# Kernel optimization log

Measured on AMD Instinct MI355X. Metric: run time of the kernel, lower is better.

Reference implementation:

```python
import jax, jax.numpy as jnp
import numpy as np
from jax import lax

V_PATCH = (1, 2, 3, 4, 5, 6, 8, 10, 13, 16)
BETA = 0.25
RESI = 0.5          # abs(quant_resi): h*(1-r) + conv(h)*r
K_PHI = 4           # share_quant_resi
PHI_TICKS = np.linspace(1.0 / (3 * K_PHI), 1.0 - 1.0 / (3 * K_PHI), K_PHI)


def _area_mat(out_s, in_s):
    # torch F.interpolate(mode='area') == adaptive avg pool: row-stochastic matrix
    M = np.zeros((out_s, in_s), np.float32)
    for i in range(out_s):
        s = (i * in_s) // out_s
        e = -((-(i + 1) * in_s) // out_s)  # ceil((i+1)*in/out)
        M[i, s:e] = 1.0 / (e - s)
    return jnp.asarray(M)


def _bicubic_mat(out_s, in_s):
    # torch bicubic, align_corners=False, a=-0.75, border-clamped taps
    a = -0.75
    i = np.arange(out_s)
    src = (i + 0.5) * in_s / out_s - 0.5
    fl = np.floor(src)
    M = np.zeros((out_s, in_s), np.float32)
    for t in range(-1, 3):
        x = np.abs(src - (fl + t))
        w = np.where(x <= 1.0, (a + 2) * x**3 - (a + 3) * x**2 + 1.0,
                     np.where(x < 2.0, a * x**3 - 5 * a * x**2 + 8 * a * x - 4 * a, 0.0))
        idx = np.clip(fl + t, 0, in_s - 1).astype(int)
        np.add.at(M, (i, idx), w)
    return jnp.asarray(M)


def _resize(x, M):
    # separable resize on square maps: x [B,C,h,w] -> [B,C,o,o]
    x = jnp.einsum('oh,bchw->bcow', M, x)
    return jnp.einsum('pw,bcow->bcop', M, x)


def _phi(h, w, b):
    # Phi: Conv2d(C,C,3,pad=1); out = h*(1-r) + conv(h)*r
    c = lax.conv_general_dilated(h, w, (1, 1), 'SAME',
                                 dimension_numbers=('NCHW', 'OIHW', 'NCHW'))
    c = c + b[None, :, None, None]
    return h * (1.0 - RESI) + c * RESI


def setup_inputs() -> dict:
    key = jax.random.key(0)
    k1, k2, k3, k4 = jax.random.split(key, 4)
    f = jax.random.normal(k1, (128, 32, 16, 16), jnp.float32)
    emb = jax.random.normal(k2, (4096, 32), jnp.float32) * 0.1
    phi_w = jax.random.normal(k3, (4, 32, 32, 3, 3), jnp.float32) * 0.05
    phi_b = jax.random.normal(k4, (4, 32), jnp.float32) * 0.01
    return {"f_BChw": f, "emb_W": emb, "phi_W": phi_w, "phi_b": phi_b}


def reference(f_BChw, emb_W, phi_W, phi_b):
    B, C, H, W = f_BChw.shape
    SN = len(V_PATCH)
    f = f_BChw.astype(jnp.float32)
    f_ng = lax.stop_gradient(f)
    f_rest = f_ng
    f_hat = jnp.zeros_like(f_ng)
    emb_ng = lax.stop_gradient(emb_W)         # torch uses embedding.weight.data
    e_sq = jnp.sum(emb_ng**2, axis=1)          # [V]
    loss = jnp.float32(0.0)
    idx_list = []
    for si, pn in enumerate(V_PATCH):
        rest = f_rest if si == SN - 1 else _resize(f_rest, _area_mat(pn, H))
        rest_NC = rest.transpose(0, 2, 3, 1).reshape(-1, C)      # [B*pn*pn, C]
        d = jnp.sum(rest_NC**2, axis=1, keepdims=True) + e_sq - 2.0 * (rest_NC @ emb_ng.T)
        idx = jnp.argmin(d, axis=1)                              # [B*pn*pn]
        idx_list.append(idx)
        h = emb_W[idx].reshape(B, pn, pn, C).transpose(0, 3, 1, 2)  # differentiable gather
        if si != SN - 1:
            h = _resize(h, _bicubic_mat(H, pn))
        k = int(np.argmin(np.abs(PHI_TICKS - si / (SN - 1))))
        h = _phi(h, phi_W[k], phi_b[k])
        f_hat = f_hat + h
        f_rest = f_rest - h
        loss = loss + BETA * jnp.mean((lax.stop_gradient(f_hat) - f)**2) \
                    + jnp.mean((f_hat - f_ng)**2)
    loss = loss / SN
    f_hat_out = lax.stop_gradient(f_hat) - f_ng + f  # straight-through
    return (f_hat_out, loss, jnp.concatenate(idx_list))
```

## Files before the change

kernel.cpp:

```cpp
#include <hip/hip_runtime.h>
#include <hip/hip_bf16.h>
#include <math.h>


#define B_  128
#define V_  4096
#define SN_ 10
#define NPIX_ (B_*32*256)

#define WS_FREST   0
#define WS_PD      1048576
#define WS_PI      1310720
#define WS_ESQ     1572864
#define WS_TW      1576960
#define WS_TI      1577536
#define WS_LOSSP   1578112
#define WS_RESTH   1580672
#define WS_RESTM   2104960
#define WS_RESTL   2629248
#define WS_EMBH    3153536
#define WS_EMBM    3219072
#define WS_EMBL    3284608
#define WS_WSPL    3350144

typedef __attribute__((ext_vector_type(8))) short short8_t;
typedef __attribute__((ext_vector_type(4))) float f32x4;
#define MFMA(a,b,c) __builtin_amdgcn_mfma_f32_16x16x32_bf16((a),(b),(c),0,0,0)

__device__ inline void gl_lds16(const void* g, void* l) {
  __builtin_amdgcn_global_load_lds((const __attribute__((address_space(1))) void*)g,
                                   (__attribute__((address_space(3))) void*)l, 16, 0, 0);
}
__device__ inline void gl_lds4(const void* g, void* l) {
  __builtin_amdgcn_global_load_lds((const __attribute__((address_space(1))) void*)g,
                                   (__attribute__((address_space(3))) void*)l, 4, 0, 0);
}

__device__ inline void split3(float a, ushort* h, ushort* m, ushort* l) {
  unsigned ua = __float_as_uint(a);
  ushort uh = (ushort)(ua >> 16);
  float fh = __uint_as_float((unsigned)uh << 16);
  float r1 = a - fh;
  ushort um = (ushort)(__float_as_uint(r1) >> 16);
  float fm = __uint_as_float((unsigned)um << 16);
  float r2 = r1 - fm;
  ushort ul = (ushort)(__float_as_uint(r2) >> 16);
  *h = uh; *m = um; *l = ul;
}

__device__ inline short8_t s8_from_laneM1(short8_t v) {
  union { short8_t s; unsigned u[4]; } a, r;
  a.s = v;
#pragma unroll
  for (int i = 0; i < 4; ++i)
    r.u[i] = __builtin_amdgcn_update_dpp(0u, a.u[i], 0x111, 0xF, 0xF, true);
  return r.s;
}
__device__ inline short8_t s8_from_laneP1(short8_t v) {
  union { short8_t s; unsigned u[4]; } a, r;
  a.s = v;
#pragma unroll
  for (int i = 0; i < 4; ++i)
    r.u[i] = __builtin_amdgcn_update_dpp(0u, a.u[i], 0x101, 0xF, 0xF, true);
  return r.s;
}


__global__ __launch_bounds__(256) void k_prep(const float* __restrict__ emb,
                                              const float* __restrict__ f,
                                              const float* __restrict__ phiW,
                                              float* __restrict__ esq,
                                              ushort* __restrict__ eh,
                                              ushort* __restrict__ em,
                                              ushort* __restrict__ el,
                                              float* __restrict__ tw,
                                              int* __restrict__ ti,
                                              ushort* __restrict__ rh,
                                              ushort* __restrict__ rm,
                                              ushort* __restrict__ rl,
                                              ushort* __restrict__ wspl) {
  int bx = blockIdx.x, t = threadIdx.x;
  if (bx < 16) {
    int v = bx * 256 + t;
    const float4* e4 = (const float4*)(emb + (size_t)v * 32);
    float s = 0.f;
#pragma unroll
    for (int half = 0; half < 4; ++half) {
      float4 x0 = e4[half * 2], x1 = e4[half * 2 + 1];
      s += x0.x * x0.x + x0.y * x0.y + x0.z * x0.z + x0.w * x0.w;
      s += x1.x * x1.x + x1.y * x1.y + x1.z * x1.z + x1.w * x1.w;
      float xs[8] = {x0.x, x0.y, x0.z, x0.w, x1.x, x1.y, x1.z, x1.w};
      ushort hs[8], ms[8], ls[8];
#pragma unroll
      for (int j = 0; j < 8; ++j) split3(xs[j], &hs[j], &ms[j], &ls[j]);
      uint4 ph, pm, pl;
      ph.x = (unsigned)hs[0] | ((unsigned)hs[1] << 16); ph.y = (unsigned)hs[2] | ((unsigned)hs[3] << 16);
      ph.z = (unsigned)hs[4] | ((unsigned)hs[5] << 16); ph.w = (unsigned)hs[6] | ((unsigned)hs[7] << 16);
      pm.x = (unsigned)ms[0] | ((unsigned)ms[1] << 16); pm.y = (unsigned)ms[2] | ((unsigned)ms[3] << 16);
      pm.z = (unsigned)ms[4] | ((unsigned)ms[5] << 16); pm.w = (unsigned)ms[6] | ((unsigned)ms[7] << 16);
      pl.x = (unsigned)ls[0] | ((unsigned)ls[1] << 16); pl.y = (unsigned)ls[2] | ((unsigned)ls[3] << 16);
      pl.z = (unsigned)ls[4] | ((unsigned)ls[5] << 16); pl.w = (unsigned)ls[6] | ((unsigned)ls[7] << 16);
      ((uint4*)(eh + (size_t)v * 32))[half] = ph;
      ((uint4*)(em + (size_t)v * 32))[half] = pm;
      ((uint4*)(el + (size_t)v * 32))[half] = pl;
    }
    esq[v] = -0.5f * s;
  } else if (bx == 16) {
    if (t >= 144) return;
    const int pns[9] = {1, 2, 3, 4, 5, 6, 8, 10, 13};
    int si = t / 16, Y = t % 16;
    int pn = pns[si];
    double src = (Y + 0.5) * (double)pn / 16.0 - 0.5;
    double fl = floor(src);
    const double a = -0.75;
#pragma unroll
    for (int k = 0; k < 4; ++k) {
      double x = fabs(src - (fl + (k - 1)));
      double w;
      if (x <= 1.0)      w = (a + 2.0) * x * x * x - (a + 3.0) * x * x + 1.0;
      else if (x < 2.0)  w = a * x * x * x - 5.0 * a * x * x + 8.0 * a * x - 4.0 * a;
      else               w = 0.0;
      int id = (int)fl + (k - 1);
      id = id < 0 ? 0 : (id > pn - 1 ? pn - 1 : id);
      tw[si * 64 + Y * 4 + k] = (float)w;
      ti[si * 64 + Y * 4 + k] = id;
    }
  } else if (bx < 33) {
    int i = (bx - 17) * 256 + t;
    int phi = i >> 10, o = (i >> 5) & 31, ci = i & 31;
    const float* src = phiW + (((size_t)phi * 32 + o) * 32 + ci) * 9;
    ushort* dst = wspl + (size_t)phi * 27648;
#pragma unroll
    for (int q = 0; q < 9; ++q) {
      ushort uh, um, ul;
      split3(src[q], &uh, &um, &ul);
      dst[(size_t)(0 * 9 + q) * 1024 + o * 32 + ci] = uh;
      dst[(size_t)(9 + q) * 1024 + o * 32 + ci] = um;
      dst[(size_t)(18 + q) * 1024 + o * 32 + ci] = ul;
    }
  } else {
    int tid = (bx - 33) * 256 + t;
    int c = tid & 31, n = tid >> 5;
    const float* base = f + ((size_t)n * 32 + c) * 256;
    float s = 0.f;
    for (int yy = 0; yy < 16; ++yy)
      for (int xx = 0; xx < 16; ++xx) s += base[yy * 16 + xx];
    float a = s * ((1.0f / 16.0f) * (1.0f / 16.0f));
    ushort uh, um, ul;
    split3(a, &uh, &um, &ul);
    rh[(size_t)n * 32 + c] = uh;
    rm[(size_t)n * 32 + c] = um;
    rl[(size_t)n * 32 + c] = ul;
  }
}

template<int R>
__global__ __launch_bounds__(256) void k_nn(const ushort* __restrict__ rest_h,
                                            const ushort* __restrict__ rest_m,
                                            const ushort* __restrict__ rest_l,
                                            const ushort* __restrict__ emb_h,
                                            const ushort* __restrict__ emb_m,
                                            const ushort* __restrict__ emb_l,
                                            const float* __restrict__ esq_g,
                                            float* __restrict__ pdist,
                                            int* __restrict__ pidx,
                                            int rows, int S, int cps) {
  __shared__ ushort lb[3][3][2048];
  __shared__ float les[3][64];
  const int t = threadIdx.x;
  const int w = t >> 6;
  const int col = t & 15;
  const int g = (t >> 4) & 3;
  const int sp = blockIdx.y;
  const int rowbase = blockIdx.x * (64 * R);

  auto stage = [&](int bf, int ch) {
    int cb = sp * cps + ch * 64;
    int code = cb + (t >> 2);
    int u = (t & 3) ^ ((code ^ (code >> 2)) & 3);
    size_t off = (size_t)code * 32 + (size_t)u * 8;
    gl_lds16(emb_h + off, &lb[bf][0][w * 512]);
    gl_lds16(emb_m + off, &lb[bf][1][w * 512]);
    gl_lds16(emb_l + off, &lb[bf][2][w * 512]);
    if ((t & 63) < 16) gl_lds4(esq_g + cb + w * 16 + (t & 15), &les[bf][w * 16]);
  };

  const int NC = cps >> 6;
  stage(0, 0);

  short8_t ah[R], am[R], al[R];
#pragma unroll
  for (int rt = 0; rt < R; ++rt) {
    int n = rowbase + (w * R + rt) * 16 + col;
    if (n >= rows) n = rows - 1;
    size_t o = (size_t)n * 32 + g * 8;
    ah[rt] = *(const short8_t*)(rest_h + o);
    am[rt] = *(const short8_t*)(rest_m + o);
    al[rt] = *(const short8_t*)(rest_l + o);
  }

  if (NC > 1) stage(1, 1);

  float best[R][4];
  int bidx[R][4];
#pragma unroll
  for (int rt = 0; rt < R; ++rt)
#pragma unroll
    for (int r = 0; r < 4; ++r) { best[rt][r] = -3.4e38f; bidx[rt][r] = 0x7fffffff; }

  int buf = 0;
  for (int ch = 0; ch < NC; ++ch) {
    if (ch + 2 < NC) {
      stage((ch + 2) % 3, ch + 2);
      asm volatile("s_waitcnt vmcnt(8)" ::: "memory");
    } else if (ch + 1 < NC) {
      asm volatile("s_waitcnt vmcnt(4)" ::: "memory");
    } else {
      asm volatile("s_waitcnt vmcnt(0)" ::: "memory");
    }
    __builtin_amdgcn_s_barrier();

    int cb0 = sp * cps + ch * 64;
#pragma unroll
    for (int s4 = 0; s4 < 4; ++s4) {
      int cl = s4 * 16 + col;
      int slotbase = (cl * 4 + (g ^ ((cl ^ (cl >> 2)) & 3))) * 8;
      short8_t bh  = *(const short8_t*)&lb[buf][0][slotbase];
      short8_t bm  = *(const short8_t*)&lb[buf][1][slotbase];
      short8_t bl2 = *(const short8_t*)&lb[buf][2][slotbase];
      float es = les[buf][cl];
      f32x4 c0 = {es, es, es, es};
      f32x4 acc[R];
#pragma unroll
      for (int rt = 0; rt < R; ++rt) acc[rt] = MFMA(ah[rt], bh, c0);
#pragma unroll
      for (int rt = 0; rt < R; ++rt) acc[rt] = MFMA(ah[rt], bm, acc[rt]);
#pragma unroll
      for (int rt = 0; rt < R; ++rt) acc[rt] = MFMA(am[rt], bh, acc[rt]);
#pragma unroll
      for (int rt = 0; rt < R; ++rt) acc[rt] = MFMA(ah[rt], bl2, acc[rt]);
#pragma unroll
      for (int rt = 0; rt < R; ++rt) acc[rt] = MFMA(am[rt], bm, acc[rt]);
#pragma unroll
      for (int rt = 0; rt < R; ++rt) acc[rt] = MFMA(al[rt], bh, acc[rt]);
      int code = cb0 + cl;
#pragma unroll
      for (int rt = 0; rt < R; ++rt)
#pragma unroll
        for (int r = 0; r < 4; ++r)
          if (acc[rt][r] > best[rt][r]) { best[rt][r] = acc[rt][r]; bidx[rt][r] = code; }
    }
    __syncthreads();
    buf = (buf + 1) % 3;
  }

#pragma unroll
  for (int rt = 0; rt < R; ++rt)
#pragma unroll
    for (int r = 0; r < 4; ++r) {
      float bd = best[rt][r];
      int bi = bidx[rt][r];
#pragma unroll
      for (int mm2 = 1; mm2 < 16; mm2 <<= 1) {
        float od = __shfl_xor(bd, mm2, 16);
        int oi = __shfl_xor(bi, mm2, 16);
        if (od > bd || (od == bd && oi < bi)) { bd = od; bi = oi; }
      }
      if ((t & 15) == 0) {
        int rown = rowbase + (w * R + rt) * 16 + g * 4 + r;
        if (rown < rows) {
          pdist[(size_t)rown * S + sp] = bd;
          pidx[(size_t)rown * S + sp] = bi;
        }
      }
    }
}

template<bool LAST>
__global__ __launch_bounds__(512) void k_scale(const float* __restrict__ pdist,
                                               const int* __restrict__ pidx,
                                               const float* __restrict__ emb,
                                               const float* __restrict__ tw,
                                               const int* __restrict__ ti,
                                               const ushort* __restrict__ wspl,
                                               const float* __restrict__ bias,
                                               const float* __restrict__ f,
                                               const float* __restrict__ fr_in,
                                               float* __restrict__ fr_out,
                                               float* __restrict__ fhat_out,
                                               float* __restrict__ out_idx_f,
                                               float* __restrict__ lossp,
                                               ushort* __restrict__ rh,
                                               ushort* __restrict__ rm,
                                               ushort* __restrict__ rl,
                                               int S, int pn, int si, int pn_next) {
  __shared__ ushort h_bf[3][256][40];
  __shared__ float xt[32][208];
  __shared__ float h_my[16][260];
  __shared__ int ci_s[256];
  __shared__ float redw[8];
  float* hsm = (float*)&h_bf[0][0][0];
  float* poolb = &xt[0][0];

  const int b = blockIdx.x;
  const int cog = blockIdx.y * 16;
  const int t = threadIdx.x;
  const int pn2 = pn * pn;

  for (int rem = t; rem < pn2; rem += 512) {
    const float* pd = pdist + (size_t)(b * pn2 + rem) * S;
    const int* pi = pidx + (size_t)(b * pn2 + rem) * S;
    float bd = pd[0]; int bi = pi[0];
    for (int s = 1; s < S; ++s) {
      float d = pd[s]; int i2 = pi[s];
      if (d > bd || (d == bd && i2 < bi)) { bd = d; bi = i2; }
    }
    ci_s[rem] = bi;
    out_idx_f[b * pn2 + rem] = (float)bi;
  }
  __syncthreads();

  if (LAST) {
    for (int i = t; i < 8192; i += 512) {
      int pix = i & 255, c = i >> 8;
      float v = emb[(size_t)ci_s[pix] * 32 + c];
      ushort uh, um, ul; split3(v, &uh, &um, &ul);
      h_bf[0][pix][c] = uh; h_bf[1][pix][c] = um; h_bf[2][pix][c] = ul;
      int cl = c - cog;
      if ((unsigned)cl < 16u) h_my[cl][pix] = v;
    }
  } else {
    for (int i = t; i < 32 * pn2; i += 512) {
      int c = i & 31, rem = i >> 5;
      hsm[c * 176 + rem] = emb[(size_t)ci_s[rem] * 32 + c];
    }
    __syncthreads();
    int e1 = 32 * pn * 16;
    for (int i = t; i < e1; i += 512) {
      int X = i & 15, r2 = i >> 4;
      int y = r2 % pn, c = r2 / pn;
      float a = 0.f;
#pragma unroll
      for (int u = 0; u < 4; ++u)
        a += tw[si * 64 + X * 4 + u] * hsm[c * 176 + y * pn + ti[si * 64 + X * 4 + u]];
      xt[c][y * 16 + X] = a;
    }
    __syncthreads();
    for (int i = t; i < 8192; i += 512) {
      int pix = i & 255, c = i >> 8;
      int X = pix & 15, Y = pix >> 4;
      float a = 0.f;
#pragma unroll
      for (int u = 0; u < 4; ++u)
        a += tw[si * 64 + Y * 4 + u] * xt[c][ti[si * 64 + Y * 4 + u] * 16 + X];
      ushort uh, um, ul; split3(a, &uh, &um, &ul);
      h_bf[0][pix][c] = uh; h_bf[1][pix][c] = um; h_bf[2][pix][c] = ul;
      int cl = c - cog;
      if ((unsigned)cl < 16u) h_my[cl][pix] = a;
    }
  }
  __syncthreads();

  const int w = t >> 6, l = t & 63;
  const int X = l & 15, kq = l >> 4;

  float fr_old[2][4], f_old[2][4];
#pragma unroll
  for (int rr = 0; rr < 2; ++rr) {
    int pix = (w * 2 + rr) * 16 + X;
#pragma unroll
    for (int r = 0; r < 4; ++r) {
      size_t ga = ((size_t)b * 32 + cog + kq * 4 + r) * 256 + pix;
      fr_old[rr][r] = fr_in[ga];
      f_old[rr][r] = LAST ? f[ga] : 0.f;
    }
  }

  f32x4 accA[2], accB[2];
#pragma unroll
  for (int r = 0; r < 4; ++r) {
    float bv = bias[cog + kq * 4 + r];
    accA[0][r] = bv; accA[1][r] = bv;
    accB[0][r] = 0.f; accB[1][r] = 0.f;
  }

  for (int dy = 0; dy < 3; ++dy) {
    short8_t bc[2][3];
    bool ok0, ok1;
    {
      int Yp = w * 2 + 0 + dy - 1;
      ok0 = (Yp >= 0 && Yp < 16);
      if (ok0) {
#pragma unroll
        for (int lv = 0; lv < 3; ++lv)
          bc[0][lv] = *(const short8_t*)&h_bf[lv][Yp * 16 + X][kq * 8];
      }
    }
    {
      int Yp = w * 2 + 1 + dy - 1;
      ok1 = (Yp >= 0 && Yp < 16);
      if (ok1) {
#pragma unroll
        for (int lv = 0; lv < 3; ++lv)
          bc[1][lv] = *(const short8_t*)&h_bf[lv][Yp * 16 + X][kq * 8];
      }
    }
#pragma unroll
    for (int dx = 0; dx < 3; ++dx) {
      int q = dy * 3 + dx;
      const ushort* wp = wspl + (size_t)q * 1024 + (size_t)(cog + (l & 15)) * 32 + kq * 8;
      short8_t aH = *(const short8_t*)(wp);
      short8_t aM = *(const short8_t*)(wp + 9 * 1024);
      short8_t aL = *(const short8_t*)(wp + 18 * 1024);
#pragma unroll
      for (int rr = 0; rr < 2; ++rr) {
        bool ok = rr ? ok1 : ok0;
        if (!ok) continue;
        short8_t bH = bc[rr][0], bM = bc[rr][1], bL = bc[rr][2];
        if (dx == 0) { bH = s8_from_laneM1(bH); bM = s8_from_laneM1(bM); bL = s8_from_laneM1(bL); }
        else if (dx == 2) { bH = s8_from_laneP1(bH); bM = s8_from_laneP1(bM); bL = s8_from_laneP1(bL); }
        accA[rr] = MFMA(aH, bH, accA[rr]);
        accB[rr] = MFMA(aH, bM, accB[rr]);
        accA[rr] = MFMA(aM, bH, accA[rr]);
        accB[rr] = MFMA(aH, bL, accB[rr]);
        accA[rr] = MFMA(aM, bM, accA[rr]);
        accB[rr] = MFMA(aL, bH, accB[rr]);
      }
    }
  }

  float lsum = 0.f;
#pragma unroll
  for (int rr = 0; rr < 2; ++rr) {
    int pix = (w * 2 + rr) * 16 + X;
#pragma unroll
    for (int r = 0; r < 4; ++r) {
      int ol = kq * 4 + r;
      float convv = accA[rr][r] + accB[rr][r];
      float outv = 0.5f * h_my[ol][pix] + 0.5f * convv;
      float nf = fr_old[rr][r] - outv;
      size_t ga = ((size_t)b * 32 + cog + ol) * 256 + pix;
      if (LAST) {
        fhat_out[ga] = f_old[rr][r] - nf;
      } else {
        fr_out[ga] = nf;
        poolb[ol * 256 + pix] = nf;
      }
      lsum += nf * nf;
    }
  }

  if (!LAST) {
    __syncthreads();
    int pn2n = pn_next * pn_next;
    for (int i = t; i < 16 * pn2n; i += 512) {
      int o = i / pn2n, rem = i - o * pn2n;
      int y = rem / pn_next, x = rem - y * pn_next;
      int sy = (y * 16) / pn_next, ey = ((y + 1) * 16 + pn_next - 1) / pn_next;
      int sx = (x * 16) / pn_next, ex = ((x + 1) * 16 + pn_next - 1) / pn_next;
      float s = 0.f;
      for (int yy = sy; yy < ey; ++yy)
        for (int xx = sx; xx < ex; ++xx) s += poolb[o * 256 + yy * 16 + xx];
      float a = s * ((1.0f / (float)(ey - sy)) * (1.0f / (float)(ex - sx)));
      ushort uh, um, ul;
      split3(a, &uh, &um, &ul);
      size_t n = (size_t)b * pn2n + rem;
      rh[n * 32 + cog + o] = uh;
      rm[n * 32 + cog + o] = um;
      rl[n * 32 + cog + o] = ul;
    }
  }

#pragma unroll
  for (int off = 32; off > 0; off >>= 1) lsum += __shfl_down(lsum, off);
  if (l == 0) redw[w] = lsum;
  __syncthreads();
  if (t == 0) {
    float s2 = 0.f;
#pragma unroll
    for (int i = 0; i < 8; ++i) s2 += redw[i];
    lossp[si * 256 + blockIdx.y * 128 + b] = s2;
  }
}

__global__ __launch_bounds__(256) void k_lossfin(const float* __restrict__ part,
                                                 float* __restrict__ out) {
  int t = threadIdx.x;
  float s = 0.f;
  for (int i = t; i < SN_ * 256; i += 256) s += part[i];
  __shared__ float red[256];
  red[t] = s;
  __syncthreads();
  for (int o = 128; o > 0; o >>= 1) {
    if (t < o) red[t] += red[t + o];
    __syncthreads();
  }
  if (t == 0) out[NPIX_] = red[0] * (1.25f / (10.0f * (float)NPIX_));
}


static void compute_phi_k(int* ks) {
  const int K = 4;
  double start = 1.0 / (3.0 * K);
  double stop = 1.0 - 1.0 / (3.0 * K);
  double step = (stop - start) / (K - 1);
  double ticks[4];
  for (int i = 0; i < K; ++i) ticks[i] = (double)i * step + start;
  ticks[K - 1] = stop;
  for (int si = 0; si < SN_; ++si) {
    double x = (double)si / (SN_ - 1);
    int best = 0;
    double bd = fabs(ticks[0] - x);
    for (int i = 1; i < K; ++i) {
      double d = fabs(ticks[i] - x);
      if (d < bd) { bd = d; best = i; }
    }
    ks[si] = best;
  }
}

extern "C" void kernel_launch(void* const* d_in, const int* in_sizes, int n_in,
                              void* d_out, int out_size, void* d_ws, size_t ws_size,
                              hipStream_t stream) {
  (void)in_sizes; (void)n_in; (void)out_size; (void)ws_size;
  const float* f    = (const float*)d_in[0];
  const float* emb  = (const float*)d_in[1];
  const float* phiW = (const float*)d_in[2];
  const float* phiB = (const float*)d_in[3];
  float* out = (float*)d_out;
  float* ws = (float*)d_ws;

  float* f_rest = ws + WS_FREST;
  float* pdist  = ws + WS_PD;
  int*   pidx   = (int*)(ws + WS_PI);
  float* esq    = ws + WS_ESQ;
  float* tw     = ws + WS_TW;
  int*   ti     = (int*)(ws + WS_TI);
  float* lossp  = ws + WS_LOSSP;
  ushort* rest_h = (ushort*)(ws + WS_RESTH);
  ushort* rest_m = (ushort*)(ws + WS_RESTM);
  ushort* rest_l = (ushort*)(ws + WS_RESTL);
  ushort* emb_h  = (ushort*)(ws + WS_EMBH);
  ushort* emb_m  = (ushort*)(ws + WS_EMBM);
  ushort* emb_l  = (ushort*)(ws + WS_EMBL);
  ushort* wspl   = (ushort*)(ws + WS_WSPL);

  static const int pns[SN_] = {1, 2, 3, 4, 5, 6, 8, 10, 13, 16};
  static const int Rs[SN_]  = {1, 1, 1, 2, 2, 2, 4, 4, 4, 4};
  static const int Ss[SN_]  = {64, 64, 32, 32, 32, 16, 16, 16, 8, 8};
  int ks[SN_];
  compute_phi_k(ks);

  k_prep<<<49, 256, 0, stream>>>(emb, f, phiW, esq, emb_h, emb_m, emb_l, tw, ti,
                                 rest_h, rest_m, rest_l, wspl);

  int idx_off = 0;
  for (int si = 0; si < SN_; ++si) {
    int pn = pns[si];
    int pn2 = pn * pn;
    int rows = B_ * pn2;
    int R = Rs[si], S = Ss[si];
    int cps = V_ / S;
    int rowblocks = (rows + 64 * R - 1) / (64 * R);

    dim3 grid(rowblocks, S);
    if (R == 1)
      k_nn<1><<<grid, 256, 0, stream>>>(rest_h, rest_m, rest_l, emb_h, emb_m, emb_l,
                                        esq, pdist, pidx, rows, S, cps);
    else if (R == 2)
      k_nn<2><<<grid, 256, 0, stream>>>(rest_h, rest_m, rest_l, emb_h, emb_m, emb_l,
                                        esq, pdist, pidx, rows, S, cps);
    else
      k_nn<4><<<grid, 256, 0, stream>>>(rest_h, rest_m, rest_l, emb_h, emb_m, emb_l,
                                        esq, pdist, pidx, rows, S, cps);

    bool last = (si == SN_ - 1);
    int pn_next = last ? 0 : pns[si + 1];
    const ushort* wsp = wspl + (size_t)ks[si] * 27648;
    const float* bi = phiB + (size_t)ks[si] * 32;
    if (last)
      k_scale<true><<<dim3(B_, 2), 512, 0, stream>>>(
          pdist, pidx, emb, tw, ti, wsp, bi, f,
          f_rest, f_rest, out,
          out + NPIX_ + 1 + idx_off, lossp,
          rest_h, rest_m, rest_l, S, pn, si, pn_next);
    else
      k_scale<false><<<dim3(B_, 2), 512, 0, stream>>>(
          pdist, pidx, emb, tw, ti, wsp, bi, f,
          (si == 0) ? f : f_rest, f_rest, nullptr,
          out + NPIX_ + 1 + idx_off, lossp,
          rest_h, rest_m, rest_l, S, pn, si, pn_next);
    idx_off += rows;
  }

  k_lossfin<<<1, 256, 0, stream>>>(lossp, out);
}
```

Measured before the change: 425.3 us.

## Widen k_scale to 1024 threads, stage conv weights in LDS, raise NN splits

k_scale now runs 1024 threads, with one image row per wave instead of two. The 3x3 conv weight slices for the block's 16 output channels are staged once into LDS rather than re-read from global memory inside the dy/dx loop. The nearest-neighbour kernel uses more codebook splits (S) and smaller R at mid scales, which raises grid parallelism, and it raises wave priority around the MFMA chain. The risks are larger partial-result buffers (the workspace layout is shifted to fit them), more LDS per block, and extra partial entries to reduce in k_scale.

Result: slower. 463.5 us (+9.0%).

```diff
diff --git a/kernel.cpp b/kernel.cpp
--- a/kernel.cpp
+++ b/kernel.cpp
@@ -10,18 +10,18 @@
 
 #define WS_FREST   0
 #define WS_PD      1048576
-#define WS_PI      1310720
-#define WS_ESQ     1572864
-#define WS_TW      1576960
-#define WS_TI      1577536
-#define WS_LOSSP   1578112
-#define WS_RESTH   1580672
-#define WS_RESTM   2104960
-#define WS_RESTL   2629248
-#define WS_EMBH    3153536
-#define WS_EMBM    3219072
-#define WS_EMBL    3284608
-#define WS_WSPL    3350144
+#define WS_PI      1572864
+#define WS_ESQ     2097152
+#define WS_TW      2101248
+#define WS_TI      2101824
+#define WS_LOSSP   2102400
+#define WS_RESTH   2105344
+#define WS_RESTM   2629632
+#define WS_RESTL   3153920
+#define WS_EMBH    3678208
+#define WS_EMBM    3743744
+#define WS_EMBL    3809280
+#define WS_WSPL    3874816
 
 typedef __attribute__((ext_vector_type(8))) short short8_t;
 typedef __attribute__((ext_vector_type(4))) float f32x4;
@@ -231,6 +231,7 @@
       float es = les[buf][cl];
       f32x4 c0 = {es, es, es, es};
       f32x4 acc[R];
+      __builtin_amdgcn_s_setprio(1);
 #pragma unroll
       for (int rt = 0; rt < R; ++rt) acc[rt] = MFMA(ah[rt], bh, c0);
 #pragma unroll
@@ -243,6 +244,7 @@
       for (int rt = 0; rt < R; ++rt) acc[rt] = MFMA(am[rt], bm, acc[rt]);
 #pragma unroll
       for (int rt = 0; rt < R; ++rt) acc[rt] = MFMA(al[rt], bh, acc[rt]);
+      __builtin_amdgcn_s_setprio(0);
       int code = cb0 + cl;
 #pragma unroll
       for (int rt = 0; rt < R; ++rt)
@@ -277,28 +279,29 @@
 }
 
 template<bool LAST>
-__global__ __launch_bounds__(512) void k_scale(const float* __restrict__ pdist,
-                                               const int* __restrict__ pidx,
-                                               const float* __restrict__ emb,
-                                               const float* __restrict__ tw,
-                                               const int* __restrict__ ti,
-                                               const ushort* __restrict__ wspl,
-                                               const float* __restrict__ bias,
-                                               const float* __restrict__ f,
-                                               const float* __restrict__ fr_in,
-                                               float* __restrict__ fr_out,
-                                               float* __restrict__ fhat_out,
-                                               float* __restrict__ out_idx_f,
-                                               float* __restrict__ lossp,
-                                               ushort* __restrict__ rh,
-                                               ushort* __restrict__ rm,
-                                               ushort* __restrict__ rl,
-                                               int S, int pn, int si, int pn_next) {
+__global__ __launch_bounds__(1024) void k_scale(const float* __restrict__ pdist,
+                                                const int* __restrict__ pidx,
+                                                const float* __restrict__ emb,
+                                                const float* __restrict__ tw,
+                                                const int* __restrict__ ti,
+                                                const ushort* __restrict__ wspl,
+                                                const float* __restrict__ bias,
+                                                const float* __restrict__ f,
+                                                const float* __restrict__ fr_in,
+                                                float* __restrict__ fr_out,
+                                                float* __restrict__ fhat_out,
+                                                float* __restrict__ out_idx_f,
+                                                float* __restrict__ lossp,
+                                                ushort* __restrict__ rh,
+                                                ushort* __restrict__ rm,
+                                                ushort* __restrict__ rl,
+                                                int S, int pn, int si, int pn_next) {
   __shared__ ushort h_bf[3][256][40];
   __shared__ float xt[32][208];
   __shared__ float h_my[16][260];
+  __shared__ ushort w_lds[27][16][36];
   __shared__ int ci_s[256];
-  __shared__ float redw[8];
+  __shared__ float redw[16];
   float* hsm = (float*)&h_bf[0][0][0];
   float* poolb = &xt[0][0];
 
@@ -307,7 +310,15 @@
   const int t = threadIdx.x;
   const int pn2 = pn * pn;
 
-  for (int rem = t; rem < pn2; rem += 512) {
+  for (int i = t; i < 1728; i += 1024) {
+    int seg = i & 3;
+    int o = (i >> 2) & 15;
+    int lq = i >> 6;
+    const ushort* src = wspl + ((size_t)lq * 32 + cog + o) * 32 + seg * 8;
+    *(short8_t*)&w_lds[lq][o][seg * 8] = *(const short8_t*)src;
+  }
+
+  for (int rem = t; rem < pn2; rem += 1024) {
     const float* pd = pdist + (size_t)(b * pn2 + rem) * S;
     const int* pi = pidx + (size_t)(b * pn2 + rem) * S;
     float bd = pd[0]; int bi = pi[0];
@@ -321,7 +332,7 @@
   __syncthreads();
 
   if (LAST) {
-    for (int i = t; i < 8192; i += 512) {
+    for (int i = t; i < 8192; i += 1024) {
       int pix = i & 255, c = i >> 8;
       float v = emb[(size_t)ci_s[pix] * 32 + c];
       ushort uh, um, ul; split3(v, &uh, &um, &ul);
@@ -330,13 +341,13 @@
       if ((unsigned)cl < 16u) h_my[cl][pix] = v;
     }
   } else {
-    for (int i = t; i < 32 * pn2; i += 512) {
+    for (int i = t; i < 32 * pn2; i += 1024) {
       int c = i & 31, rem = i >> 5;
       hsm[c * 176 + rem] = emb[(size_t)ci_s[rem] * 32 + c];
     }
     __syncthreads();
     int e1 = 32 * pn * 16;
-    for (int i = t; i < e1; i += 512) {
+    for (int i = t; i < e1; i += 1024) {
       int X = i & 15, r2 = i >> 4;
       int y = r2 % pn, c = r2 / pn;
       float a = 0.f;
@@ -346,7 +357,7 @@
       xt[c][y * 16 + X] = a;
     }
     __syncthreads();
-    for (int i = t; i < 8192; i += 512) {
+    for (int i = t; i < 8192; i += 1024) {
       int pix = i & 255, c = i >> 8;
       int X = pix & 15, Y = pix >> 4;
       float a = 0.f;
@@ -363,97 +374,72 @@
 
   const int w = t >> 6, l = t & 63;
   const int X = l & 15, kq = l >> 4;
-
-  float fr_old[2][4], f_old[2][4];
-#pragma unroll
-  for (int rr = 0; rr < 2; ++rr) {
-    int pix = (w * 2 + rr) * 16 + X;
-#pragma unroll
-    for (int r = 0; r < 4; ++r) {
-      size_t ga = ((size_t)b * 32 + cog + kq * 4 + r) * 256 + pix;
-      fr_old[rr][r] = fr_in[ga];
-      f_old[rr][r] = LAST ? f[ga] : 0.f;
-    }
-  }
-
-  f32x4 accA[2], accB[2];
+  const int pix = w * 16 + X;
+
+  float fr_old[4], f_old[4];
 #pragma unroll
   for (int r = 0; r < 4; ++r) {
-    float bv = bias[cog + kq * 4 + r];
-    accA[0][r] = bv; accA[1][r] = bv;
-    accB[0][r] = 0.f; accB[1][r] = 0.f;
+    size_t ga = ((size_t)b * 32 + cog + kq * 4 + r) * 256 + pix;
+    fr_old[r] = fr_in[ga];
+    f_old[r] = LAST ? f[ga] : 0.f;
+  }
+
+  f32x4 accA, accB;
+#pragma unroll
+  for (int r = 0; r < 4; ++r) {
+    accA[r] = bias[cog + kq * 4 + r];
+    accB[r] = 0.f;
   }
 
   for (int dy = 0; dy < 3; ++dy) {
-    short8_t bc[2][3];
-    bool ok0, ok1;
-    {
-      int Yp = w * 2 + 0 + dy - 1;
-      ok0 = (Yp >= 0 && Yp < 16);
-      if (ok0) {
-#pragma unroll
-        for (int lv = 0; lv < 3; ++lv)
-          bc[0][lv] = *(const short8_t*)&h_bf[lv][Yp * 16 + X][kq * 8];
-      }
-    }
-    {
-      int Yp = w * 2 + 1 + dy - 1;
-      ok1 = (Yp >= 0 && Yp < 16);
-      if (ok1) {
-#pragma unroll
-        for (int lv = 0; lv < 3; ++lv)
-          bc[1][lv] = *(const short8_t*)&h_bf[lv][Yp * 16 + X][kq * 8];
-      }
+    int Yp = w + dy - 1;
+    bool ok = (Yp >= 0 && Yp < 16);
+    short8_t bc[3];
+    if (ok) {
+#pragma unroll
+      for (int lv = 0; lv < 3; ++lv)
+        bc[lv] = *(const short8_t*)&h_bf[lv][Yp * 16 + X][kq * 8];
     }
 #pragma unroll
     for (int dx = 0; dx < 3; ++dx) {
       int q = dy * 3 + dx;
-      const ushort* wp = wspl + (size_t)q * 1024 + (size_t)(cog + (l & 15)) * 32 + kq * 8;
-      short8_t aH = *(const short8_t*)(wp);
-      short8_t aM = *(const short8_t*)(wp + 9 * 1024);
-      short8_t aL = *(const short8_t*)(wp + 18 * 1024);
-#pragma unroll
-      for (int rr = 0; rr < 2; ++rr) {
-        bool ok = rr ? ok1 : ok0;
-        if (!ok) continue;
-        short8_t bH = bc[rr][0], bM = bc[rr][1], bL = bc[rr][2];
-        if (dx == 0) { bH = s8_from_laneM1(bH); bM = s8_from_laneM1(bM); bL = s8_from_laneM1(bL); }
-        else if (dx == 2) { bH = s8_from_laneP1(bH); bM = s8_from_laneP1(bM); bL = s8_from_laneP1(bL); }
-        accA[rr] = MFMA(aH, bH, accA[rr]);
-        accB[rr] = MFMA(aH, bM, accB[rr]);
-        accA[rr] = MFMA(aM, bH, accA[rr]);
-        accB[rr] = MFMA(aH, bL, accB[rr]);
-        accA[rr] = MFMA(aM, bM, accA[rr]);
-        accB[rr] = MFMA(aL, bH, accB[rr]);
-      }
+      short8_t aH = *(const short8_t*)&w_lds[0 * 9 + q][l & 15][kq * 8];
+      short8_t aM = *(const short8_t*)&w_lds[9 + q][l & 15][kq * 8];
+      short8_t aL = *(const short8_t*)&w_lds[18 + q][l & 15][kq * 8];
+      if (!ok) continue;
+      short8_t bH = bc[0], bM = bc[1], bL = bc[2];
+      if (dx == 0) { bH = s8_from_laneM1(bH); bM = s8_from_laneM1(bM); bL = s8_from_laneM1(bL); }
+      else if (dx == 2) { bH = s8_from_laneP1(bH); bM = s8_from_laneP1(bM); bL = s8_from_laneP1(bL); }
+      accA = MFMA(aH, bH, accA);
+      accB = MFMA(aH, bM, accB);
+      accA = MFMA(aM, bH, accA);
+      accB = MFMA(aH, bL, accB);
+      accA = MFMA(aM, bM, accA);
+      accB = MFMA(aL, bH, accB);
     }
   }
 
   float lsum = 0.f;
 #pragma unroll
-  for (int rr = 0; rr < 2; ++rr) {
-    int pix = (w * 2 + rr) * 16 + X;
-#pragma unroll
-    for (int r = 0; r < 4; ++r) {
-      int ol = kq * 4 + r;
-      float convv = accA[rr][r] + accB[rr][r];
-      float outv = 0.5f * h_my[ol][pix] + 0.5f * convv;
-      float nf = fr_old[rr][r] - outv;
-      size_t ga = ((size_t)b * 32 + cog + ol) * 256 + pix;
-      if (LAST) {
-        fhat_out[ga] = f_old[rr][r] - nf;
-      } else {
-        fr_out[ga] = nf;
-        poolb[ol * 256 + pix] = nf;
-      }
-      lsum += nf * nf;
-    }
+  for (int r = 0; r < 4; ++r) {
+    int ol = kq * 4 + r;
+    float convv = accA[r] + accB[r];
+    float outv = 0.5f * h_my[ol][pix] + 0.5f * convv;
+    float nf = fr_old[r] - outv;
+    size_t ga = ((size_t)b * 32 + cog + ol) * 256 + pix;
+    if (LAST) {
+      fhat_out[ga] = f_old[r] - nf;
+    } else {
+      fr_out[ga] = nf;
+      poolb[ol * 256 + pix] = nf;
+    }
+    lsum += nf * nf;
   }
 
   if (!LAST) {
     __syncthreads();
     int pn2n = pn_next * pn_next;
-    for (int i = t; i < 16 * pn2n; i += 512) {
+    for (int i = t; i < 16 * pn2n; i += 1024) {
       int o = i / pn2n, rem = i - o * pn2n;
       int y = rem / pn_next, x = rem - y * pn_next;
       int sy = (y * 16) / pn_next, ey = ((y + 1) * 16 + pn_next - 1) / pn_next;
@@ -478,7 +464,7 @@
   if (t == 0) {
     float s2 = 0.f;
 #pragma unroll
-    for (int i = 0; i < 8; ++i) s2 += redw[i];
+    for (int i = 0; i < 16; ++i) s2 += redw[i];
     lossp[si * 256 + blockIdx.y * 128 + b] = s2;
   }
 }
@@ -546,8 +532,8 @@
   ushort* wspl   = (ushort*)(ws + WS_WSPL);
 
   static const int pns[SN_] = {1, 2, 3, 4, 5, 6, 8, 10, 13, 16};
-  static const int Rs[SN_]  = {1, 1, 1, 2, 2, 2, 4, 4, 4, 4};
-  static const int Ss[SN_]  = {64, 64, 32, 32, 32, 16, 16, 16, 8, 8};
+  static const int Rs[SN_]  = {1, 1, 1, 1, 2, 2, 4, 4, 4, 4};
+  static const int Ss[SN_]  = {64, 64, 64, 64, 64, 64, 32, 32, 16, 16};
   int ks[SN_];
   compute_phi_k(ks);
 
@@ -579,13 +565,13 @@
     const ushort* wsp = wspl + (size_t)ks[si] * 27648;
     const float* bi = phiB + (size_t)ks[si] * 32;
     if (last)
-      k_scale<true><<<dim3(B_, 2), 512, 0, stream>>>(
+      k_scale<true><<<dim3(B_, 2), 1024, 0, stream>>>(
           pdist, pidx, emb, tw, ti, wsp, bi, f,
           f_rest, f_rest, out,
           out + NPIX_ + 1 + idx_off, lossp,
           rest_h, rest_m, rest_l, S, pn, si, pn_next);
     else
-      k_scale<false><<<dim3(B_, 2), 512, 0, stream>>>(
+      k_scale<false><<<dim3(B_, 2), 1024, 0, stream>>>(
           pdist, pidx, emb, tw, ti, wsp, bi, f,
           (si == 0) ? f : f_rest, f_rest, nullptr,
           out + NPIX_ + 1 + idx_off, lossp,
```
